# Performance work log

Measured on AMD Instinct MI355X. Metric: run time of the kernel, lower is better.

## Reference

```python
import jax, jax.numpy as jnp
import numpy as np

S, B, I, H, L, D = 512, 64, 128, 256, 6, 2  # seq, batch, input, hidden, layers, directions


def setup_inputs() -> dict:
    key = jax.random.key(0)
    ks = jax.random.split(key, 7)
    stdv = 1.0 / np.sqrt(H)
    u = lambda k, shape: jax.random.uniform(k, shape, jnp.float32, -stdv, stdv)
    return {
        "x": jax.random.normal(ks[0], (S, B, I), jnp.float32),
        "h0": jax.random.normal(ks[1], (L * D, B, H), jnp.float32),
        "w_ih0": u(ks[2], (D, 3 * H, I)),            # layer 0 input weights
        "w_ih": u(ks[3], (L - 1, D, 3 * H, D * H)),  # layers 1.. input weights
        "w_hh": u(ks[4], (L, D, 3 * H, H)),
        "b_ih": u(ks[5], (L, D, 3 * H)),
        "b_hh": u(ks[6], (L, D, 3 * H)),
    }


def _gru_direction(gate_x, w_hh, b_hh, h0, reverse):
    # gate_x: (S, B, 3H) precomputed x @ W_ih.T + b_ih; scan the recurrence.
    def step(h, gx):
        gh = h @ w_hh.T + b_hh  # (B, 3H)
        x_r, x_z, x_n = jnp.split(gx, 3, axis=-1)
        h_r, h_z, h_n = jnp.split(gh, 3, axis=-1)
        r = jax.nn.sigmoid(x_r + h_r)
        z = jax.nn.sigmoid(x_z + h_z)
        n = jnp.tanh(x_n + r * h_n)
        h_new = (1.0 - z) * n + z * h
        return h_new, h_new

    h_last, ys = jax.lax.scan(step, h0, gate_x, reverse=reverse)
    return h_last, ys  # ys aligned with input time order even when reverse=True


def reference(x, h0, w_ih0, w_ih, w_hh, b_ih, b_hh):
    num_layers = w_hh.shape[0]
    inp = x  # (S, B, in_dim)
    h_n = []
    for layer in range(num_layers):
        outs = []
        for d in range(2):
            w = w_ih0[d] if layer == 0 else w_ih[layer - 1, d]
            # Single GEMM over the whole sequence for the input gates.
            gate_x = jnp.einsum('sbi,gi->sbg', inp, w) + b_ih[layer, d]
            h_last, ys = _gru_direction(
                gate_x, w_hh[layer, d], b_hh[layer, d],
                h0[layer * 2 + d], reverse=(d == 1))
            outs.append(ys)
            h_n.append(h_last)
        inp = jnp.concatenate(outs, axis=-1)  # (S, B, 2H)
    return jnp.stack(h_n)  # (L*2, B, H)
```

## Files before the change

kernel.cpp:

```cpp
#include <hip/hip_runtime.h>
#include <stdint.h>

#define S_LEN 512
#define NB    64
#define HID   256
#define G3    768
#define SB    32768
#define NLAYER 6

typedef short bf16x8 __attribute__((ext_vector_type(8)));
typedef short bf16x4 __attribute__((ext_vector_type(4)));
typedef float floatx4 __attribute__((ext_vector_type(4)));
typedef unsigned short u16;
typedef unsigned int   u32;

__device__ __forceinline__ float bf2f(u16 v) {
  u32 u = ((u32)v) << 16;
  return __builtin_bit_cast(float, u);
}
__device__ __forceinline__ u16 f2bf(float f) {
  u32 u = __builtin_bit_cast(u32, f);
  u = (u + 0x7FFFu + ((u >> 16) & 1u)) >> 16;
  return (u16)u;
}
__device__ __forceinline__ float fsigmoid(float x) {
  return __builtin_amdgcn_rcpf(1.0f + __expf(-x));
}
__device__ __forceinline__ float ftanh(float x) {
  return 1.0f - 2.0f * __builtin_amdgcn_rcpf(1.0f + __expf(x + x));
}

__device__ __forceinline__ void lds_barrier() {
  asm volatile("s_waitcnt lgkmcnt(0)\n\ts_barrier" ::: "memory");
}

__global__ void detect_fp32(const u16* __restrict__ x, int n, int* flag) {
  __shared__ int tot;
  if (threadIdx.x == 0) tot = 0;
  __syncthreads();
  int c = 0;
  for (int i = threadIdx.x; i < n; i += blockDim.x) {
    u16 v = x[i];
    if (((v >> 7) & 0xFF) == 0xFF) ++c;
  }
  atomicAdd(&tot, c);
  __syncthreads();
  if (threadIdx.x == 0) *flag = (tot > 64) ? 1 : 0;
}

__global__ void cvt(const void* __restrict__ src, u16* __restrict__ dst,
                    int n, const int* __restrict__ flag) {
  const int stride = gridDim.x * blockDim.x;
  const bool isf32 = (*flag != 0);
  for (int i = blockIdx.x * blockDim.x + threadIdx.x; i < n; i += stride) {
    if (isf32) dst[i] = f2bf(((const float*)src)[i]);
    else       dst[i] = ((const u16*)src)[i];
  }
}

__global__ void prep_bias(const u16* __restrict__ bih, const u16* __restrict__ bhh,
                          float* __restrict__ bc, int n) {
  int i = blockIdx.x * blockDim.x + threadIdx.x;
  if (i >= n) return;
  int col = i % G3;
  float v = bf2f(bih[i]);
  if (col < 512) v += bf2f(bhh[i]);
  bc[i] = v;
}

__global__ void write_out(const float* __restrict__ hNs, void* __restrict__ out,
                          int n, const int* __restrict__ flag) {
  int i = blockIdx.x * blockDim.x + threadIdx.x;
  if (i >= n) return;
  if (*flag) ((float*)out)[i] = hNs[i];
  else       ((u16*)out)[i]   = f2bf(hNs[i]);
}

__global__ __launch_bounds__(256)
void gate_gemm(const u16* __restrict__ A, const u16* __restrict__ W,
               const float* __restrict__ bias, u16* __restrict__ outg, int K) {
  const int m0  = blockIdx.x * 128;
  const int n0  = blockIdx.y * 128;
  const int dir = blockIdx.z;
  W    += (size_t)dir * G3 * K;
  bias += (size_t)dir * G3;
  outg += (size_t)dir * (size_t)SB * G3;

  __shared__ __align__(16) u16 lA[8192];
  __shared__ __align__(16) u16 lB[8192];

  const int tid  = threadIdx.x;
  const int lane = tid & 63;
  const int wv   = tid >> 6;
  const int wm   = wv & 1, wn = wv >> 1;
  const int l15  = lane & 15, quad = lane >> 4;

  floatx4 acc[4][4] = {};

  for (int k0 = 0; k0 < K; k0 += 64) {
    bf16x8 ra[4], rb[4];
#pragma unroll
    for (int i = 0; i < 4; ++i) {
      int c   = i * 256 + tid;
      int row = c >> 3;
      int kc  = (c & 7) ^ (row & 7);
      ra[i] = *(const bf16x8*)(A + (size_t)(m0 + row) * K + (k0 + kc * 8));
      rb[i] = *(const bf16x8*)(W + (size_t)(n0 + row) * K + (k0 + kc * 8));
    }
    __syncthreads();
#pragma unroll
    for (int i = 0; i < 4; ++i) {
      *(bf16x8*)(lA + (size_t)(i * 256 + tid) * 8) = ra[i];
      *(bf16x8*)(lB + (size_t)(i * 256 + tid) * 8) = rb[i];
    }
    __syncthreads();

#pragma unroll
    for (int kt = 0; kt < 2; ++kt) {
      bf16x8 af[4], bfr[4];
#pragma unroll
      for (int mt = 0; mt < 4; ++mt) {
        int row = wm * 64 + mt * 16 + l15;
        int ch  = row * 8 + ((kt * 4 + quad) ^ (row & 7));
        af[mt] = *(const bf16x8*)(lA + ch * 8);
      }
#pragma unroll
      for (int nt = 0; nt < 4; ++nt) {
        int row = wn * 64 + nt * 16 + l15;
        int ch  = row * 8 + ((kt * 4 + quad) ^ (row & 7));
        bfr[nt] = *(const bf16x8*)(lB + ch * 8);
      }
#pragma unroll
      for (int mt = 0; mt < 4; ++mt)
#pragma unroll
        for (int nt = 0; nt < 4; ++nt)
          acc[mt][nt] = __builtin_amdgcn_mfma_f32_16x16x32_bf16(
              af[mt], bfr[nt], acc[mt][nt], 0, 0, 0);
    }
  }

  const int sIdx = (m0 >> 6) + wm;
#pragma unroll
  for (int nt = 0; nt < 4; ++nt) {
    int n    = n0 + wn * 64 + nt * 16 + l15;
    int g    = n >> 8, jc = n & 255;
    float bv = bias[n];
#pragma unroll
    for (int mt = 0; mt < 4; ++mt) {
      bf16x4 pk;
#pragma unroll
      for (int r = 0; r < 4; ++r) pk[r] = (short)f2bf(acc[mt][nt][r] + bv);
      *(bf16x4*)(outg + ((((size_t)mt * 512 + sIdx) * 256 + jc) * 3 + g) * 16 +
                 quad * 4) = pk;
    }
  }
}

__global__ __launch_bounds__(512)
__attribute__((amdgpu_waves_per_eu(2, 2)))
void gru_scan(const u16* __restrict__ gateX,
              const u16* __restrict__ Whh,
              const u16* __restrict__ Bhh,
              const u16* __restrict__ H0,
              u16* __restrict__ layerOut,
              float* __restrict__ hNs,
              int layer) {
  const int dir = blockIdx.x & 1;
  const int bg  = blockIdx.x >> 1;
  const int tid = threadIdx.x;
  const int lane = tid & 63;
  const int wv   = tid >> 6;
  const int l15  = lane & 15, quad = lane >> 4;

  __shared__ __align__(16) u16 wnL[16384];
  __shared__ __align__(16) u16 hb2[2][4096];

  const u16* Wd = Whh + (size_t)dir * G3 * HID;

#pragma unroll
  for (int i = 0; i < 4; ++i) {
    int ci = i * 512 + tid;
    int n  = ci >> 3;
    int kc = ci & 7;
    bf16x8 v = *(const bf16x8*)(Wd + (size_t)(512 + n) * HID + (24 + kc) * 8);
    *(bf16x8*)(wnL + kc * 2048 + n * 8) = v;
  }

  bf16x8 wrz[8][2][2];
  bf16x8 wn6[6][2];
#pragma unroll
  for (int g = 0; g < 2; ++g)
#pragma unroll
    for (int nt = 0; nt < 2; ++nt) {
      int n = g * 256 + wv * 32 + nt * 16 + l15;
#pragma unroll
      for (int kt = 0; kt < 8; ++kt)
        wrz[kt][g][nt] = *(const bf16x8*)(Wd + (size_t)n * HID + kt * 32 + quad * 8);
    }
#pragma unroll
  for (int nt = 0; nt < 2; ++nt) {
    int n = 512 + wv * 32 + nt * 16 + l15;
#pragma unroll
    for (int kt = 0; kt < 6; ++kt)
      wn6[kt][nt] = *(const bf16x8*)(Wd + (size_t)n * HID + kt * 32 + quad * 8);
  }
#pragma unroll
  for (int kt = 0; kt < 8; ++kt)
#pragma unroll
    for (int g = 0; g < 2; ++g)
#pragma unroll
      for (int nt = 0; nt < 2; ++nt)
        asm volatile("" : "+v"(wrz[kt][g][nt]));
#pragma unroll
  for (int kt = 0; kt < 6; ++kt)
#pragma unroll
    for (int nt = 0; nt < 2; ++nt)
      asm volatile("" : "+v"(wn6[kt][nt]));

  float bhn[2];
#pragma unroll
  for (int nt = 0; nt < 2; ++nt)
    bhn[nt] = bf2f(Bhh[dir * G3 + 512 + wv * 32 + nt * 16 + l15]);

  const int afb = quad * 128 + l15 * 8;
  const int bnb = quad * 2048 + (wv * 32 + l15) * 8;
  int wb[2];
#pragma unroll
  for (int nt = 0; nt < 2; ++nt)
    wb[nt] = (wv * 4 + nt * 2 + (l15 >> 3)) * 128 + quad * 32 + (l15 & 7);

  {
    int row = tid >> 5, slot = tid & 31;
    const u16* hp = H0 + ((size_t)(layer * 2 + dir) * NB + bg * 16 + row) * HID + slot * 8;
    *(bf16x8*)(&hb2[0][slot * 128 + row * 8]) = *(const bf16x8*)hp;
  }

  const long sstep = dir ? -(long)(256 * 3 * 16) : (long)(256 * 3 * 16);
  const u16* xb;
  {
    const int s0 = dir ? (S_LEN - 1) : 0;
    xb = gateX + (size_t)dir * SB * G3 +
         ((((size_t)bg * 512 + s0) * 256 + (wv * 32 + l15)) * 3) * 16 + quad * 4;
  }
  bf16x4 xp[3][2];
#pragma unroll
  for (int g = 0; g < 3; ++g)
#pragma unroll
    for (int nt = 0; nt < 2; ++nt)
      xp[g][nt] = *(const bf16x4*)(xb + nt * 768 + g * 16);
  xb += sstep;

  u16* loPtr;
  {
    int row = tid >> 5, slot = tid & 31;
    const int sFirst = dir ? (S_LEN - 1) : 0;
    loPtr = layerOut + ((size_t)sFirst * NB + bg * 16 + row) * 512 +
            dir * HID + slot * 8;
  }
  const long lostep = dir ? -(long)(NB * 512) : (long)(NB * 512);

  lds_barrier();

  for (int t = 0; t < S_LEN; ++t) {
    const int cur = t & 1, nxt = cur ^ 1;

    floatx4 aR[2], aZ[2], aN[2];
    bf16x4 xn0 = xp[2][0], xn1 = xp[2][1];
#pragma unroll
    for (int nt = 0; nt < 2; ++nt)
#pragma unroll
      for (int r = 0; r < 4; ++r) {
        aR[nt][r] = bf2f((u16)xp[0][nt][r]);
        aZ[nt][r] = bf2f((u16)xp[1][nt][r]);
        aN[nt][r] = bhn[nt];
      }

#pragma unroll
    for (int g = 0; g < 3; ++g)
#pragma unroll
      for (int nt = 0; nt < 2; ++nt)
        xp[g][nt] = *(const bf16x4*)(xb + nt * 768 + g * 16);
    if (t < S_LEN - 1) xb += sstep;

    u16 hp[2][4];
#pragma unroll
    for (int nt = 0; nt < 2; ++nt)
#pragma unroll
      for (int r = 0; r < 4; ++r)
        hp[nt][r] = hb2[cur][wb[nt] + r * 8];

    if (t > 0) {
      int row = tid >> 5, slot = tid & 31;
      bf16x8 hv = *(const bf16x8*)(&hb2[cur][slot * 128 + row * 8]);
      *(bf16x8*)loPtr = hv;
      loPtr += lostep;
    }

#pragma unroll
    for (int kt = 0; kt < 8; ++kt) {
      bf16x8 af = *(const bf16x8*)(&hb2[cur][afb + kt * 512]);
      bf16x8 bn0, bn1;
      if (kt < 6) {
        bn0 = wn6[kt][0];
        bn1 = wn6[kt][1];
      } else {
        bn0 = *(const bf16x8*)(wnL + bnb + (kt - 6) * 8192);
        bn1 = *(const bf16x8*)(wnL + bnb + (kt - 6) * 8192 + 128);
      }
      aR[0] = __builtin_amdgcn_mfma_f32_16x16x32_bf16(af, wrz[kt][0][0], aR[0], 0, 0, 0);
      aR[1] = __builtin_amdgcn_mfma_f32_16x16x32_bf16(af, wrz[kt][0][1], aR[1], 0, 0, 0);
      aZ[0] = __builtin_amdgcn_mfma_f32_16x16x32_bf16(af, wrz[kt][1][0], aZ[0], 0, 0, 0);
      aZ[1] = __builtin_amdgcn_mfma_f32_16x16x32_bf16(af, wrz[kt][1][1], aZ[1], 0, 0, 0);
      aN[0] = __builtin_amdgcn_mfma_f32_16x16x32_bf16(af, bn0,           aN[0], 0, 0, 0);
      aN[1] = __builtin_amdgcn_mfma_f32_16x16x32_bf16(af, bn1,           aN[1], 0, 0, 0);
    }

#pragma unroll
    for (int nt = 0; nt < 2; ++nt) {
      const bf16x4 xn = nt ? xn1 : xn0;
#pragma unroll
      for (int r = 0; r < 4; ++r) {
        float rg = fsigmoid(aR[nt][r]);
        float zg = fsigmoid(aZ[nt][r]);
        float ng = ftanh(bf2f((u16)xn[r]) + rg * aN[nt][r]);
        float h0 = bf2f(hp[nt][r]);
        float hn = ng + zg * (h0 - ng);
        hb2[nxt][wb[nt] + r * 8] = f2bf(hn);
      }
    }

    lds_barrier();
  }

  {
    int row = tid >> 5, slot = tid & 31;
    const int sLast = dir ? 0 : (S_LEN - 1);
    bf16x8 hv = *(const bf16x8*)(&hb2[0][slot * 128 + row * 8]);
    *(bf16x8*)(layerOut + ((size_t)sLast * NB + bg * 16 + row) * 512 +
               dir * HID + slot * 8) = hv;
    float* dst = hNs + ((size_t)(layer * 2 + dir) * NB + bg * 16 + row) * HID + slot * 8;
    floatx4 v0, v1;
#pragma unroll
    for (int i = 0; i < 4; ++i) v0[i] = bf2f((u16)hv[i]);
#pragma unroll
    for (int i = 0; i < 4; ++i) v1[i] = bf2f((u16)hv[4 + i]);
    *(floatx4*)dst = v0;
    *((floatx4*)dst + 1) = v1;
  }
}

extern "C" void kernel_launch(void* const* d_in, const int* in_sizes, int n_in,
                              void* d_out, int out_size, void* d_ws, size_t ws_size,
                              hipStream_t stream) {
  (void)n_in; (void)ws_size;
  char* ws = (char*)d_ws;
  int*   flag  = (int*)ws;
  float* hNs   = (float*)(ws + 4096);
  float* biasC = (float*)(ws + 790528);
  u16*   h0C   = (u16*)(ws + (1u << 20));
  u16*   wih0C = h0C   + 196608;
  u16*   wihC  = wih0C + 196608;
  u16*   whhC  = wihC  + 3932160;
  u16*   bihC  = whhC  + 2359296;
  u16*   bhhC  = bihC  + 9216;
  u16*   gateX = (u16*)(ws + (16u  << 20));
  u16*   bufA  = (u16*)(ws + (112u << 20));
  u16*   bufB  = (u16*)(ws + (144u << 20));
  u16*   xC    = bufB;

  detect_fp32<<<1, 1024, 0, stream>>>((const u16*)d_in[0], 262144, flag);
  cvt<<<512, 256, 0, stream>>>(d_in[0], xC,    in_sizes[0], flag);
  cvt<<<256, 256, 0, stream>>>(d_in[1], h0C,   in_sizes[1], flag);
  cvt<<<256, 256, 0, stream>>>(d_in[2], wih0C, in_sizes[2], flag);
  cvt<<<512, 256, 0, stream>>>(d_in[3], wihC,  in_sizes[3], flag);
  cvt<<<512, 256, 0, stream>>>(d_in[4], whhC,  in_sizes[4], flag);
  cvt<<< 64, 256, 0, stream>>>(d_in[5], bihC,  in_sizes[5], flag);
  cvt<<< 64, 256, 0, stream>>>(d_in[6], bhhC,  in_sizes[6], flag);
  prep_bias<<<36, 256, 0, stream>>>(bihC, bhhC, biasC, NLAYER * 2 * G3);

  for (int layer = 0; layer < NLAYER; ++layer) {
    const u16* inp = (layer == 0) ? xC : ((layer & 1) ? bufA : bufB);
    u16* outBuf    = (layer & 1) ? bufB : bufA;

    const int K = (layer == 0) ? 128 : 512;
    const u16* W = (layer == 0) ? wih0C
                                : (wihC + (size_t)(layer - 1) * 2 * G3 * 512);
    dim3 grid(256, 6, 2);
    gate_gemm<<<grid, 256, 0, stream>>>(inp, W, biasC + (size_t)layer * 2 * G3,
                                        gateX, K);
    gru_scan<<<8, 512, 0, stream>>>(gateX, whhC + (size_t)layer * 2 * G3 * HID,
                                    bhhC + (size_t)layer * 2 * G3, h0C,
                                    outBuf, hNs, layer);
  }
  write_out<<<(out_size + 255) / 256, 256, 0, stream>>>(hNs, d_out, out_size, flag);
}
```

Baseline: 5.263 ms.

## Prescale GRU weights by log2e factors, keep h in registers, pack bf16 conversions

Folds the -log2(e) and 2·log2(e) factors into the input and hidden weights and biases with a new prescale kernel, so the scan's sigmoid and tanh use exp2 directly with no negation or doubling. The previous hidden state is carried in registers as packed bf16 instead of being re-read from LDS each step, and the hardware packed bf16 convert replaces manual rounding in the GEMM epilogue and the scan. Targets ALU and LDS latency on the serial recurrence critical path, at the cost of extra prescale launches and bf16 rounding of the scaled weights, which slightly changes numerics.

```diff
diff --git a/kernel.cpp b/kernel.cpp
--- a/kernel.cpp
+++ b/kernel.cpp
@@ -11,8 +11,12 @@
 typedef short bf16x8 __attribute__((ext_vector_type(8)));
 typedef short bf16x4 __attribute__((ext_vector_type(4)));
 typedef float floatx4 __attribute__((ext_vector_type(4)));
+typedef unsigned int u32x2 __attribute__((ext_vector_type(2)));
 typedef unsigned short u16;
 typedef unsigned int   u32;
+
+#define SCL_RZ  (-1.4426950408889634f)
+#define SCL_N   ( 2.8853900817779268f)
 
 __device__ __forceinline__ float bf2f(u16 v) {
   u32 u = ((u32)v) << 16;
@@ -23,11 +27,10 @@
   u = (u + 0x7FFFu + ((u >> 16) & 1u)) >> 16;
   return (u16)u;
 }
-__device__ __forceinline__ float fsigmoid(float x) {
-  return __builtin_amdgcn_rcpf(1.0f + __expf(-x));
-}
-__device__ __forceinline__ float ftanh(float x) {
-  return 1.0f - 2.0f * __builtin_amdgcn_rcpf(1.0f + __expf(x + x));
+__device__ __forceinline__ u32 pk_bf16(float lo, float hi) {
+  u32 r;
+  asm("v_cvt_pk_bf16_f32 %0, %1, %2" : "=v"(r) : "v"(lo), "v"(hi));
+  return r;
 }
 
 __device__ __forceinline__ void lds_barrier() {
@@ -58,13 +61,22 @@
   }
 }
 
+__global__ void scale_w(u16* __restrict__ w, int n, int K) {
+  int i = blockIdx.x * blockDim.x + threadIdx.x;
+  if (i >= n) return;
+  int row = (i / K) % G3;
+  float s = (row < 512) ? SCL_RZ : SCL_N;
+  w[i] = f2bf(bf2f(w[i]) * s);
+}
+
 __global__ void prep_bias(const u16* __restrict__ bih, const u16* __restrict__ bhh,
                           float* __restrict__ bc, int n) {
   int i = blockIdx.x * blockDim.x + threadIdx.x;
   if (i >= n) return;
   int col = i % G3;
   float v = bf2f(bih[i]);
-  if (col < 512) v += bf2f(bhh[i]);
+  if (col < 512) v = SCL_RZ * (v + bf2f(bhh[i]));
+  else           v = SCL_N * v;
   bc[i] = v;
 }
 
@@ -147,11 +159,11 @@
     float bv = bias[n];
 #pragma unroll
     for (int mt = 0; mt < 4; ++mt) {
-      bf16x4 pk;
-#pragma unroll
-      for (int r = 0; r < 4; ++r) pk[r] = (short)f2bf(acc[mt][nt][r] + bv);
-      *(bf16x4*)(outg + ((((size_t)mt * 512 + sIdx) * 256 + jc) * 3 + g) * 16 +
-                 quad * 4) = pk;
+      u32x2 pr;
+      pr[0] = pk_bf16(acc[mt][nt][0] + bv, acc[mt][nt][1] + bv);
+      pr[1] = pk_bf16(acc[mt][nt][2] + bv, acc[mt][nt][3] + bv);
+      *(u32x2*)(outg + ((((size_t)mt * 512 + sIdx) * 256 + jc) * 3 + g) * 16 +
+                quad * 4) = pr;
     }
   }
 }
@@ -220,7 +232,10 @@
   float bhn[2];
 #pragma unroll
   for (int nt = 0; nt < 2; ++nt)
-    bhn[nt] = bf2f(Bhh[dir * G3 + 512 + wv * 32 + nt * 16 + l15]);
+    bhn[nt] = SCL_N * bf2f(Bhh[dir * G3 + 512 + wv * 32 + nt * 16 + l15]);
+
+  const int mrow = quad * 4;
+  const int b0   = bg * 16 + mrow;
 
   const int afb = quad * 128 + l15 * 8;
   const int bnb = quad * 2048 + (wv * 32 + l15) * 8;
@@ -233,6 +248,14 @@
     int row = tid >> 5, slot = tid & 31;
     const u16* hp = H0 + ((size_t)(layer * 2 + dir) * NB + bg * 16 + row) * HID + slot * 8;
     *(bf16x8*)(&hb2[0][slot * 128 + row * 8]) = *(const bf16x8*)hp;
+  }
+  u32 hA[2], hB[2];
+#pragma unroll
+  for (int nt = 0; nt < 2; ++nt) {
+    const u16* hp0 = H0 + ((size_t)(layer * 2 + dir) * NB + b0) * HID +
+                     wv * 32 + nt * 16 + l15;
+    hA[nt] = (u32)hp0[0]       | ((u32)hp0[HID] << 16);
+    hB[nt] = (u32)hp0[2 * HID] | ((u32)hp0[3 * HID] << 16);
   }
 
   const long sstep = dir ? -(long)(256 * 3 * 16) : (long)(256 * 3 * 16);
@@ -281,13 +304,6 @@
       for (int nt = 0; nt < 2; ++nt)
         xp[g][nt] = *(const bf16x4*)(xb + nt * 768 + g * 16);
     if (t < S_LEN - 1) xb += sstep;
-
-    u16 hp[2][4];
-#pragma unroll
-    for (int nt = 0; nt < 2; ++nt)
-#pragma unroll
-      for (int r = 0; r < 4; ++r)
-        hp[nt][r] = hb2[cur][wb[nt] + r * 8];
 
     if (t > 0) {
       int row = tid >> 5, slot = tid & 31;
@@ -318,15 +334,28 @@
 #pragma unroll
     for (int nt = 0; nt < 2; ++nt) {
       const bf16x4 xn = nt ? xn1 : xn0;
+      float h0v[4];
+      h0v[0] = __builtin_bit_cast(float, hA[nt] << 16);
+      h0v[1] = __builtin_bit_cast(float, hA[nt] & 0xFFFF0000u);
+      h0v[2] = __builtin_bit_cast(float, hB[nt] << 16);
+      h0v[3] = __builtin_bit_cast(float, hB[nt] & 0xFFFF0000u);
+      float hn[4];
 #pragma unroll
       for (int r = 0; r < 4; ++r) {
-        float rg = fsigmoid(aR[nt][r]);
-        float zg = fsigmoid(aZ[nt][r]);
-        float ng = ftanh(bf2f((u16)xn[r]) + rg * aN[nt][r]);
-        float h0 = bf2f(hp[nt][r]);
-        float hn = ng + zg * (h0 - ng);
-        hb2[nxt][wb[nt] + r * 8] = f2bf(hn);
+        float rg = __builtin_amdgcn_rcpf(1.0f + __builtin_exp2f(aR[nt][r]));
+        float zg = __builtin_amdgcn_rcpf(1.0f + __builtin_exp2f(aZ[nt][r]));
+        float y  = bf2f((u16)xn[r]) + rg * aN[nt][r];
+        float ng = 1.0f - 2.0f * __builtin_amdgcn_rcpf(1.0f + __builtin_exp2f(y));
+        hn[r] = ng + zg * (h0v[r] - ng);
       }
+      u32 p01 = pk_bf16(hn[0], hn[1]);
+      u32 p23 = pk_bf16(hn[2], hn[3]);
+      hA[nt] = p01;
+      hB[nt] = p23;
+      hb2[nxt][wb[nt]]      = (u16)p01;
+      hb2[nxt][wb[nt] + 8]  = (u16)(p01 >> 16);
+      hb2[nxt][wb[nt] + 16] = (u16)p23;
+      hb2[nxt][wb[nt] + 24] = (u16)(p23 >> 16);
     }
 
     lds_barrier();
@@ -376,6 +405,9 @@
   cvt<<<512, 256, 0, stream>>>(d_in[4], whhC,  in_sizes[4], flag);
   cvt<<< 64, 256, 0, stream>>>(d_in[5], bihC,  in_sizes[5], flag);
   cvt<<< 64, 256, 0, stream>>>(d_in[6], bhhC,  in_sizes[6], flag);
+  scale_w<<<(196608  + 255) / 256, 256, 0, stream>>>(wih0C, 196608,  128);
+  scale_w<<<(3932160 + 255) / 256, 256, 0, stream>>>(wihC,  3932160, 512);
+  scale_w<<<(2359296 + 255) / 256, 256, 0, stream>>>(whhC,  2359296, 256);
   prep_bias<<<36, 256, 0, stream>>>(bihC, bhhC, biasC, NLAYER * 2 * G3);
 
   for (int layer = 0; layer < NLAYER; ++layer) {
```

New measurement: 6.807 ms. 1.29x slower.
